# Kernel optimization log

Hardware: AMD Instinct MI355X
Metric: run time of the kernel (lower is better)

The kernel has to match this reference:

```python
import jax, jax.numpy as jnp
import numpy as np

EPS = 1e-7  # reciprocal epsilon from the original code


def hippo_skew_evals(N):
    i = np.arange(N, dtype=np.float64)
    x = 2 * i + 1
    Hippo = np.sqrt(np.outer(x, x)) * np.tri(N, k=-1)  # tril(diagonal=-1)
    Skew = (Hippo - Hippo.T) / 2
    ev = np.linalg.eigvals(Skew)
    return ev[np.argsort(-ev.imag)]  # largest imag first


def setup_inputs() -> dict:
    key = jax.random.key(0)
    ks = jax.random.split(key, 6)
    B, H, L, N = 16, 512, 2048, 64
    u = jax.random.normal(ks[0], (B, H, L), dtype=jnp.float32)
    # log_dt ~ U(log(dt_min), log(dt_max)), tiled to (H, 2) (sep_dt_re_im=True)
    dt_min, dt_max = 1e-3, 1e-1
    ld = np.log(dt_min) + jax.random.uniform(ks[1], (H,)) * (np.log(dt_max) - np.log(dt_min))
    log_dt = jnp.tile(ld[:, None], (1, 2)).astype(jnp.float32)
    # Lambda: hippo_skew_evals(2N)[:N] - 0.5, stored as real (N,2)
    w = hippo_skew_evals(2 * N)[:N] - 0.5
    Lambda = jnp.stack([jnp.asarray(w.real, jnp.float32), jnp.asarray(w.imag, jnp.float32)], axis=-1)
    W = jax.random.normal(ks[2], (1, H, N, 2), dtype=jnp.float32)
    D = jax.random.normal(ks[3], (1, H), dtype=jnp.float32)
    out_weight = jax.random.normal(ks[4], (H, H), dtype=jnp.float32) * (1.0 / np.sqrt(H))
    out_bias = jax.random.uniform(ks[5], (H, 1), dtype=jnp.float32, minval=-1.0 / np.sqrt(H), maxval=1.0 / np.sqrt(H))
    return {"u": u, "log_dt": log_dt, "Lambda": Lambda, "W": W, "D": D,
            "out_weight": out_weight, "out_bias": out_bias}


def _to_c(x):
    return x[..., 0] + 1j * x[..., 1]


def dss_kernel(log_dt, Lambda, W, L):
    # log_dt: (H,2) real; Lambda: (N,2) real; W: (C,H,N,2) real
    Lam = _to_c(Lambda)                         # (N,) complex
    Wc = _to_c(W)                               # (C,H,N) complex
    # sep_dt_re_im: scale real/imag parts of Lambda by separate dt's
    dtL = jnp.exp(log_dt)[:, None, :] * Lambda[None, :, :]  # (H,N,2)
    dt_Lambda = _to_c(dtL)                      # (H,N) complex
    pos = (Lam.real > 0).astype(jnp.float32)    # (N,)
    l = jnp.arange(L, dtype=jnp.float32)
    P = dt_Lambda[..., None] * l                # (H,N,L)
    P_max = jax.lax.stop_gradient(dt_Lambda * (pos * (L - 1)))
    P = P - P_max[..., None]
    S = jnp.exp(P)                              # (H,N,L)
    dt_Lambda_neg = dt_Lambda * (1 - 2 * pos)
    num = jnp.exp(dt_Lambda_neg) - 1            # (H,N)
    den = jnp.exp(dt_Lambda_neg * L) - 1        # (H,N)
    x = den * Lam
    recip = jnp.conj(x) / (x * jnp.conj(x) + EPS)  # bounded 1/x
    Wk = Wc * num * recip                       # (C,H,N)
    # torch .float() on complex keeps real part
    return jnp.einsum('chn,hnl->chl', Wk, S).real  # (C,H,L)


def reference(u, log_dt, Lambda, W, D, out_weight, out_bias):
    # u: (B,H,L), transposed layout
    L = u.shape[-1]
    k = dss_kernel(log_dt, Lambda, W, L)        # (1,H,L)
    n_fft = 2 * L
    k_f = jnp.fft.rfft(k, n=n_fft)              # (1,H,L+1)
    u_f = jnp.fft.rfft(u, n=n_fft)              # (B,H,L+1)
    y_f = jnp.einsum('bhl,chl->bchl', u_f, k_f)
    y = jnp.fft.irfft(y_f, n=n_fft)[..., :L]    # (B,1,H,L)
    y = y + jnp.einsum('bhl,ch->bchl', u, D)    # skip connection
    B = u.shape[0]
    y = y.reshape(B, -1, L)                     # (B, C*H, L), C=1
    y = jax.nn.gelu(y, approximate=False)       # torch nn.GELU default (erf)
    # TransposedLinear: '... u l, v u -> ... v l' + bias (H,1)
    y = jnp.einsum('bul,vu->bvl', y, out_weight) + out_bias
    return y
```

## Files before the change

### kernel.cpp

```cpp
#include <hip/hip_runtime.h>
#include <hip/hip_bf16.h>
#include <math.h>

#define HH 512
#define NN 64
#define LLEN 2048
#define BB 16

typedef __attribute__((ext_vector_type(8))) short short8;
typedef __attribute__((ext_vector_type(4))) float f32x4;

#define SW(j,e) ((e) ^ (((j)&3)<<3))

__device__ inline unsigned short f2bf(float f) {
    union { float f; unsigned int u; } v; v.f = f;
    unsigned int x = v.u;
    unsigned int r = (x + 0x7fffu + ((x >> 16) & 1u)) >> 16;
    return (unsigned short)r;
}
__device__ inline float bf2f(unsigned short x) {
    union { unsigned int u; float f; } v; v.u = ((unsigned int)x) << 16;
    return v.f;
}
__device__ inline unsigned int pk_bf16(float a, float b) {
#if __has_builtin(__builtin_amdgcn_cvt_pk_bf16_f32)
    auto r = __builtin_amdgcn_cvt_pk_bf16_f32(a, b);
    unsigned int o; __builtin_memcpy(&o, &r, 4); return o;
#else
    return (unsigned int)f2bf(a) | ((unsigned int)f2bf(b) << 16);
#endif
}

__device__ inline void gload_lds16(const unsigned short* g, unsigned short* l) {
    __builtin_amdgcn_global_load_lds(
        (const __attribute__((address_space(1))) void*)g,
        (__attribute__((address_space(3))) void*)l, 16, 0, 0);
}

__global__ __launch_bounds__(256) void k_coeffs(
    const float* __restrict__ log_dt,
    const float* __restrict__ Lambda,
    const float* __restrict__ W,
    float* __restrict__ c_re,  float* __restrict__ c_im) {
    int idx = blockIdx.x * 256 + threadIdx.x;
    int h = idx >> 6, n = idx & 63;
    float lre = Lambda[n * 2 + 0], lim = Lambda[n * 2 + 1];
    float dtr = expf(log_dt[h * 2 + 0]);
    float dti = expf(log_dt[h * 2 + 1]);
    float ar = dtr * lre;
    float ai = dti * lim;
    float pos = (lre > 0.0f) ? 1.0f : 0.0f;
    float pm = pos * (float)(LLEN - 1);
    float er = expf(-ar * pm);
    float epr = er * cosf(-ai * pm), epi = er * sinf(-ai * pm);
    float sgn = 1.0f - 2.0f * pos;
    float nr = ar * sgn, ni = ai * sgn;
    float en = expf(nr);
    float numr = en * cosf(ni) - 1.0f, numi = en * sinf(ni);
    float eL = expf(nr * (float)LLEN);
    float denr = eL * cosf(ni * (float)LLEN) - 1.0f;
    float deni = eL * sinf(ni * (float)LLEN);
    float xr = denr * lre - deni * lim;
    float xi = denr * lim + deni * lre;
    float d = xr * xr + xi * xi + 1e-7f;
    float rr = xr / d, ri = -xi / d;
    float wr = W[(h * 64 + n) * 2 + 0], wi = W[(h * 64 + n) * 2 + 1];
    float t1r = wr * numr - wi * numi;
    float t1i = wr * numi + wi * numr;
    float wkr = t1r * rr - t1i * ri;
    float wki = t1r * ri + t1i * rr;
    c_re[idx] = wkr * epr - wki * epi;
    c_im[idx] = wkr * epi + wki * epr;
}

__global__ __launch_bounds__(256) void k_w2b(const float* __restrict__ w,
                                             unsigned short* __restrict__ wb) {
    int idx = blockIdx.x * 256 + threadIdx.x;
    wb[idx] = f2bf(w[idx]);
}

__global__ __launch_bounds__(256) void k_prep(
    const float* __restrict__ log_dt, const float* __restrict__ Lambda,
    const float* __restrict__ c_re, const float* __restrict__ c_im,
    const float* __restrict__ D,
    unsigned short* __restrict__ Tm,
    unsigned short* __restrict__ Are, unsigned short* __restrict__ Aim,
    unsigned short* __restrict__ Pre, unsigned short* __restrict__ Pim,
    float2* __restrict__ lam64) {
    int h = blockIdx.x;
    int tid = threadIdx.x;
    __shared__ float ar_s[64], ai_s[64], cr_s[64], ci_s[64], k_s[64];
    if (tid < 64) {
        int n = tid;
        float dtr = expf(log_dt[h * 2 + 0]);
        float dti = expf(log_dt[h * 2 + 1]);
        float ar = dtr * Lambda[n * 2 + 0];
        float ai = dti * Lambda[n * 2 + 1];
        ar_s[n] = ar; ai_s[n] = ai;
        cr_s[n] = c_re[h * 64 + n]; ci_s[n] = c_im[h * 64 + n];
        float e64 = expf(64.f * ar);
        lam64[h * 64 + n] = make_float2(e64 * cosf(64.f * ai), e64 * sinf(64.f * ai));
    }
    __syncthreads();
    size_t base = (size_t)h * 4096;
#pragma unroll 4
    for (int e = 0; e < 16; ++e) {
        int idx = e * 256 + tid;
        int r = idx >> 6, q = idx & 63;
        {
            float fi = (float)(63 - q);
            float w = expf(fi * ar_s[r]);
            Are[base + idx] = f2bf(w * cosf(fi * ai_s[r]));
            Aim[base + idx] = f2bf(w * sinf(fi * ai_s[r]));
        }
        {
            float t = (float)(r + 1);
            float w = expf(t * ar_s[q]);
            float pr = w * cosf(t * ai_s[q]), pii = w * sinf(t * ai_s[q]);
            Pre[base + idx] = f2bf(cr_s[q] * pr - ci_s[q] * pii);
            Pim[base + idx] = f2bf(-(cr_s[q] * pii + ci_s[q] * pr));
        }
    }
    if (tid < 64) {
        float fd = (float)tid, acc = 0.f;
        for (int n = 0; n < 64; ++n) {
            float w = expf(fd * ar_s[n]);
            acc += cr_s[n] * (w * cosf(fd * ai_s[n])) - ci_s[n] * (w * sinf(fd * ai_s[n]));
        }
        if (tid == 0) acc += D[h];
        k_s[tid] = acc;
    }
    __syncthreads();
#pragma unroll 4
    for (int e = 0; e < 16; ++e) {
        int idx = e * 256 + tid;
        int i = idx >> 6, ip = idx & 63;
        Tm[base + idx] = (ip <= i) ? f2bf(k_s[i - ip]) : (unsigned short)0;
    }
}

__global__ __launch_bounds__(64) void k_scan2(
    const float* __restrict__ u,
    const unsigned short* __restrict__ Tm,
    const unsigned short* __restrict__ Are, const unsigned short* __restrict__ Aim,
    const unsigned short* __restrict__ Pre, const unsigned short* __restrict__ Pim,
    const float2* __restrict__ lam64,
    unsigned short* __restrict__ G) {
    __shared__ unsigned short Sre[32 * 72];
    __shared__ unsigned short Sim_[32 * 72];
    int ln = threadIdx.x;
    int sub = ln & 15, quad = ln >> 4;
    int bh = blockIdx.x;
    int h = bh >> 4, b = bh & 15;
    const float* up = u + ((size_t)b * HH + h) * LLEN;
    unsigned short* Gp = G + ((size_t)b * HH + h) * LLEN;
    size_t mb = (size_t)h * 4096;

    short8 ufr[2][2];
#pragma unroll
    for (int kc = 0; kc < 2; ++kc)
#pragma unroll
        for (int nt = 0; nt < 2; ++nt) {
            int l = (nt * 16 + sub) * 64 + kc * 32 + quad * 8;
            float4 v0 = *(const float4*)(up + l);
            float4 v1 = *(const float4*)(up + l + 4);
            union { short8 s; uint4 u4; } q;
            q.u4 = make_uint4(pk_bf16(v0.x, v0.y), pk_bf16(v0.z, v0.w),
                              pk_bf16(v1.x, v1.y), pk_bf16(v1.z, v1.w));
            ufr[kc][nt] = q.s;
        }

    f32x4 vr[4][2], vi[4][2];
#pragma unroll
    for (int mt = 0; mt < 4; ++mt)
#pragma unroll
        for (int nt = 0; nt < 2; ++nt) {
            vr[mt][nt] = (f32x4){0.f, 0.f, 0.f, 0.f};
            vi[mt][nt] = (f32x4){0.f, 0.f, 0.f, 0.f};
        }
#pragma unroll
    for (int kc = 0; kc < 2; ++kc) {
#pragma unroll
        for (int mt = 0; mt < 4; ++mt) {
            size_t ab = mb + (size_t)(mt * 16 + sub) * 64 + kc * 32 + quad * 8;
            short8 ar8 = *(const short8*)(Are + ab);
            short8 ai8 = *(const short8*)(Aim + ab);
            vr[mt][0] = __builtin_amdgcn_mfma_f32_16x16x32_bf16(ar8, ufr[kc][0], vr[mt][0], 0, 0, 0);
            vr[mt][1] = __builtin_amdgcn_mfma_f32_16x16x32_bf16(ar8, ufr[kc][1], vr[mt][1], 0, 0, 0);
            vi[mt][0] = __builtin_amdgcn_mfma_f32_16x16x32_bf16(ai8, ufr[kc][0], vi[mt][0], 0, 0, 0);
            vi[mt][1] = __builtin_amdgcn_mfma_f32_16x16x32_bf16(ai8, ufr[kc][1], vi[mt][1], 0, 0, 0);
        }
    }
#pragma unroll
    for (int mt = 0; mt < 4; ++mt)
#pragma unroll
        for (int nt = 0; nt < 2; ++nt) {
            int jj = nt * 16 + sub;
            int e0 = mt * 16 + quad * 4;
            uint2 pr, pi;
            pr.x = pk_bf16(vr[mt][nt][0], vr[mt][nt][1]);
            pr.y = pk_bf16(vr[mt][nt][2], vr[mt][nt][3]);
            pi.x = pk_bf16(vi[mt][nt][0], vi[mt][nt][1]);
            pi.y = pk_bf16(vi[mt][nt][2], vi[mt][nt][3]);
            *(uint2*)&Sre[jj * 72 + SW(jj, e0)] = pr;
            *(uint2*)&Sim_[jj * 72 + SW(jj, e0)] = pi;
        }
    __syncthreads();

    {
        float2 l64 = lam64[(size_t)h * 64 + ln];
        float sr = 0.f, si = 0.f;
        for (int j = 0; j < 32; ++j) {
            int a = j * 72 + SW(j, ln);
            float vrr = bf2f(Sre[a]);
            float vii = bf2f(Sim_[a]);
            unsigned int p = pk_bf16(sr, si);
            Sre[a] = (unsigned short)(p & 0xffffu);
            Sim_[a] = (unsigned short)(p >> 16);
            float nr = fmaf(l64.x, sr, fmaf(-l64.y, si, vrr));
            float ni = fmaf(l64.y, sr, fmaf(l64.x, si, vii));
            sr = nr; si = ni;
        }
    }
    __syncthreads();

    f32x4 y[4][2];
#pragma unroll
    for (int mt = 0; mt < 4; ++mt)
#pragma unroll
        for (int nt = 0; nt < 2; ++nt) y[mt][nt] = (f32x4){0.f, 0.f, 0.f, 0.f};
#pragma unroll
    for (int kc = 0; kc < 2; ++kc) {
        int eo = kc * 32 + quad * 8;
        short8 bsr0 = *(const short8*)&Sre[sub * 72 + SW(sub, eo)];
        short8 bsr1 = *(const short8*)&Sre[(16 + sub) * 72 + SW(16 + sub, eo)];
        short8 bsi0 = *(const short8*)&Sim_[sub * 72 + SW(sub, eo)];
        short8 bsi1 = *(const short8*)&Sim_[(16 + sub) * 72 + SW(16 + sub, eo)];
#pragma unroll
        for (int mt = 0; mt < 4; ++mt) {
            size_t ab = mb + (size_t)(mt * 16 + sub) * 64 + eo;
            short8 at8 = *(const short8*)(Tm + ab);
            short8 pr8 = *(const short8*)(Pre + ab);
            short8 pi8 = *(const short8*)(Pim + ab);
            y[mt][0] = __builtin_amdgcn_mfma_f32_16x16x32_bf16(at8, ufr[kc][0], y[mt][0], 0, 0, 0);
            y[mt][1] = __builtin_amdgcn_mfma_f32_16x16x32_bf16(at8, ufr[kc][1], y[mt][1], 0, 0, 0);
            y[mt][0] = __builtin_amdgcn_mfma_f32_16x16x32_bf16(pr8, bsr0, y[mt][0], 0, 0, 0);
            y[mt][1] = __builtin_amdgcn_mfma_f32_16x16x32_bf16(pr8, bsr1, y[mt][1], 0, 0, 0);
            y[mt][0] = __builtin_amdgcn_mfma_f32_16x16x32_bf16(pi8, bsi0, y[mt][0], 0, 0, 0);
            y[mt][1] = __builtin_amdgcn_mfma_f32_16x16x32_bf16(pi8, bsi1, y[mt][1], 0, 0, 0);
        }
    }
    __syncthreads();

#pragma unroll
    for (int mt = 0; mt < 4; ++mt)
#pragma unroll
        for (int nt = 0; nt < 2; ++nt) {
            int jj = nt * 16 + sub;
            int e0 = mt * 16 + quad * 4;
            float g[4];
#pragma unroll
            for (int r = 0; r < 4; ++r) {
                float yv = y[mt][nt][r];
                g[r] = 0.5f * yv * (1.0f + erff(yv * 0.70710678118654752f));
            }
            uint2 p;
            p.x = pk_bf16(g[0], g[1]);
            p.y = pk_bf16(g[2], g[3]);
            *(uint2*)&Sre[jj * 72 + SW(jj, e0)] = p;
        }
    __syncthreads();

    for (int t = 0; t < 4; ++t) {
        int l = t * 512 + ln * 8;
        int j = l >> 6, i = l & 63;
        uint4 q = *(const uint4*)&Sre[j * 72 + SW(j, i)];
        *(uint4*)(Gp + l) = q;
    }
}

__global__ __launch_bounds__(256) void k_tr(const unsigned short* __restrict__ G,
                                            unsigned short* __restrict__ Gt) {
    __shared__ unsigned short T[64 * 72];
    int tid = threadIdx.x;
    int l0 = blockIdx.x * 64, u0 = blockIdx.y * 64, b = blockIdx.z;
    {
        int ur = tid >> 2, ls = (tid & 3) * 16;
        const unsigned short* src = G + ((size_t)(b * HH + u0 + ur)) * LLEN + l0 + ls;
        *(uint4*)&T[ur * 72 + ls]     = *(const uint4*)(src);
        *(uint4*)&T[ur * 72 + ls + 8] = *(const uint4*)(src + 8);
    }
    __syncthreads();
    {
        int lr = tid >> 2, us = (tid & 3) * 16;
        unsigned short tmp[16];
#pragma unroll
        for (int k2 = 0; k2 < 16; ++k2) tmp[k2] = T[(us + k2) * 72 + lr];
        unsigned short* dst = Gt + ((size_t)(b * LLEN + l0 + lr)) * HH + u0 + us;
        *(uint4*)(dst)     = *(uint4*)&tmp[0];
        *(uint4*)(dst + 8) = *(uint4*)&tmp[8];
    }
}

__global__ __launch_bounds__(256) void k_proj(
    const unsigned short* __restrict__ Gt,
    const unsigned short* __restrict__ Wb,
    const float* __restrict__ bias,
    float* __restrict__ out) {
    __shared__ unsigned short As[128 * 64];
    __shared__ unsigned short Bs[128 * 64];
    int tid = threadIdx.x;
    int w = tid >> 6, ln = tid & 63;
    int wm = w & 1, wn = w >> 1;
    int quad = ln >> 4, sub = ln & 15;
    int v0 = blockIdx.x * 128, l0 = blockIdx.y * 128, b = blockIdx.z;
    int r_in = ln >> 3, cch = ln & 7;
    int gch = cch ^ r_in;

    f32x4 acc[4][4];
#pragma unroll
    for (int mt = 0; mt < 4; ++mt)
#pragma unroll
        for (int nt = 0; nt < 4; ++nt) acc[mt][nt] = (f32x4){0.f, 0.f, 0.f, 0.f};

    for (int k0 = 0; k0 < HH; k0 += 64) {
        __syncthreads();
#pragma unroll
        for (int i = 0; i < 4; ++i) {
            int row = w * 32 + i * 8 + r_in;
            const unsigned short* ga = Wb + (size_t)(v0 + row) * HH + k0 + gch * 8;
            gload_lds16(ga, &As[(w * 32 + i * 8) * 64]);
            const unsigned short* gb = Gt + ((size_t)(b * LLEN + l0 + row)) * HH + k0 + gch * 8;
            gload_lds16(gb, &Bs[(w * 32 + i * 8) * 64]);
        }
        __syncthreads();
#pragma unroll
        for (int kc = 0; kc < 2; ++kc) {
            int ch = (kc * 4 + quad) ^ (sub & 7);
            short8 af[4], bf[4];
#pragma unroll
            for (int mt = 0; mt < 4; ++mt)
                af[mt] = *(const short8*)&As[(wm * 64 + mt * 16 + sub) * 64 + ch * 8];
#pragma unroll
            for (int nt = 0; nt < 4; ++nt)
                bf[nt] = *(const short8*)&Bs[(wn * 64 + nt * 16 + sub) * 64 + ch * 8];
#pragma unroll
            for (int mt = 0; mt < 4; ++mt)
#pragma unroll
                for (int nt = 0; nt < 4; ++nt)
                    acc[mt][nt] = __builtin_amdgcn_mfma_f32_16x16x32_bf16(af[mt], bf[nt], acc[mt][nt], 0, 0, 0);
        }
    }
#pragma unroll
    for (int mt = 0; mt < 4; ++mt) {
#pragma unroll
        for (int i = 0; i < 4; ++i) {
            int v = v0 + wm * 64 + mt * 16 + quad * 4 + i;
            float bv = bias[v];
#pragma unroll
            for (int nt = 0; nt < 4; ++nt) {
                int l = l0 + wn * 64 + nt * 16 + sub;
                out[((size_t)b * HH + v) * LLEN + l] = acc[mt][nt][i] + bv;
            }
        }
    }
}

extern "C" void kernel_launch(void* const* d_in, const int* in_sizes, int n_in,
                              void* d_out, int out_size, void* d_ws, size_t ws_size,
                              hipStream_t stream) {
    const float* u       = (const float*)d_in[0];
    const float* log_dt  = (const float*)d_in[1];
    const float* Lambda  = (const float*)d_in[2];
    const float* W       = (const float*)d_in[3];
    const float* D       = (const float*)d_in[4];
    const float* out_w   = (const float*)d_in[5];
    const float* out_b   = (const float*)d_in[6];
    float* out = (float*)d_out;

    char* ws = (char*)d_ws;
    float* c_re   = (float*)(ws + 0);
    float* c_im   = (float*)(ws + 131072);
    unsigned short* Wb = (unsigned short*)(ws + 524288);
    unsigned short* G  = (unsigned short*)(ws + 1048576);
    size_t moff = 34603008;
    const size_t MSZ = (size_t)HH * 4096 * 2;
    unsigned short* TmB  = (unsigned short*)(ws + moff);
    unsigned short* AreB = (unsigned short*)(ws + moff + 1 * MSZ);
    unsigned short* AimB = (unsigned short*)(ws + moff + 2 * MSZ);
    unsigned short* PreB = (unsigned short*)(ws + moff + 3 * MSZ);
    unsigned short* PimB = (unsigned short*)(ws + moff + 4 * MSZ);
    float2* lam64B = (float2*)(ws + moff + 5 * MSZ);
    unsigned short* Gt = (unsigned short*)(ws + moff);

    hipLaunchKernelGGL(k_coeffs, dim3(128), dim3(256), 0, stream,
                       log_dt, Lambda, W, c_re, c_im);
    hipLaunchKernelGGL(k_w2b, dim3(1024), dim3(256), 0, stream, out_w, Wb);
    hipLaunchKernelGGL(k_prep, dim3(512), dim3(256), 0, stream,
                       log_dt, Lambda, c_re, c_im, D,
                       TmB, AreB, AimB, PreB, PimB, lam64B);
    hipLaunchKernelGGL(k_scan2, dim3(8192), dim3(64), 0, stream,
                       u, TmB, AreB, AimB, PreB, PimB, lam64B, G);
    hipLaunchKernelGGL(k_tr, dim3(32, 8, 16), dim3(256), 0, stream, G, Gt);
    hipLaunchKernelGGL(k_proj, dim3(4, 16, 16), dim3(256), 0, stream,
                       Gt, Wb, out_b, out);
}
```

Measured before the change: 262.9 us.

## Fuse coefficient and weight-cast kernels into prep, pack scan waves, fast GELU

Merges the coefficient and weight-to-bf16 kernels into the per-h prep kernel, so the launch sequence loses two kernels and the c_re/c_im round trip. The scan kernel now runs four independent (b,h) waves per 256-thread block with per-wave LDS slices and a new XOR-free rotation swizzle. The scan kernel also writes GELU output straight to global memory instead of staging it through LDS, and replaces erf GELU with a tanh-style approximation built on exp2 and rcp. The approximation changes numerics slightly, and the direct stores are narrower and less coalesced. The __syncthreads calls are now shared across four waves that each only touch their own slice.

```diff
diff --git a/kernel.cpp b/kernel.cpp
--- a/kernel.cpp
+++ b/kernel.cpp
@@ -9,8 +9,6 @@
 
 typedef __attribute__((ext_vector_type(8))) short short8;
 typedef __attribute__((ext_vector_type(4))) float f32x4;
-
-#define SW(j,e) ((e) ^ (((j)&3)<<3))
 
 __device__ inline unsigned short f2bf(float f) {
     union { float f; unsigned int u; } v; v.f = f;
@@ -31,75 +29,84 @@
 #endif
 }
 
+__device__ inline float fast_rcp(float x) {
+#if __has_builtin(__builtin_amdgcn_rcpf)
+    return __builtin_amdgcn_rcpf(x);
+#else
+    return 1.0f / x;
+#endif
+}
+__device__ inline float fast_exp2(float x) {
+#if __has_builtin(__builtin_amdgcn_exp2f)
+    return __builtin_amdgcn_exp2f(x);
+#else
+    return exp2f(x);
+#endif
+}
+__device__ inline float fast_gelu(float x) {
+    float x2 = x * x;
+    float t = fmaf(0.044715f, x2, 1.0f);
+    float z2 = 1.5957691216057308f * x * t;
+    float e = fast_exp2(-1.4426950408889634f * z2);
+    return x * fast_rcp(1.0f + e);
+}
+
 __device__ inline void gload_lds16(const unsigned short* g, unsigned short* l) {
     __builtin_amdgcn_global_load_lds(
         (const __attribute__((address_space(1))) void*)g,
         (__attribute__((address_space(3))) void*)l, 16, 0, 0);
 }
 
-__global__ __launch_bounds__(256) void k_coeffs(
-    const float* __restrict__ log_dt,
-    const float* __restrict__ Lambda,
-    const float* __restrict__ W,
-    float* __restrict__ c_re,  float* __restrict__ c_im) {
-    int idx = blockIdx.x * 256 + threadIdx.x;
-    int h = idx >> 6, n = idx & 63;
-    float lre = Lambda[n * 2 + 0], lim = Lambda[n * 2 + 1];
-    float dtr = expf(log_dt[h * 2 + 0]);
-    float dti = expf(log_dt[h * 2 + 1]);
-    float ar = dtr * lre;
-    float ai = dti * lim;
-    float pos = (lre > 0.0f) ? 1.0f : 0.0f;
-    float pm = pos * (float)(LLEN - 1);
-    float er = expf(-ar * pm);
-    float epr = er * cosf(-ai * pm), epi = er * sinf(-ai * pm);
-    float sgn = 1.0f - 2.0f * pos;
-    float nr = ar * sgn, ni = ai * sgn;
-    float en = expf(nr);
-    float numr = en * cosf(ni) - 1.0f, numi = en * sinf(ni);
-    float eL = expf(nr * (float)LLEN);
-    float denr = eL * cosf(ni * (float)LLEN) - 1.0f;
-    float deni = eL * sinf(ni * (float)LLEN);
-    float xr = denr * lre - deni * lim;
-    float xi = denr * lim + deni * lre;
-    float d = xr * xr + xi * xi + 1e-7f;
-    float rr = xr / d, ri = -xi / d;
-    float wr = W[(h * 64 + n) * 2 + 0], wi = W[(h * 64 + n) * 2 + 1];
-    float t1r = wr * numr - wi * numi;
-    float t1i = wr * numi + wi * numr;
-    float wkr = t1r * rr - t1i * ri;
-    float wki = t1r * ri + t1i * rr;
-    c_re[idx] = wkr * epr - wki * epi;
-    c_im[idx] = wkr * epi + wki * epr;
-}
-
-__global__ __launch_bounds__(256) void k_w2b(const float* __restrict__ w,
-                                             unsigned short* __restrict__ wb) {
-    int idx = blockIdx.x * 256 + threadIdx.x;
-    wb[idx] = f2bf(w[idx]);
-}
-
-__global__ __launch_bounds__(256) void k_prep(
+__global__ __launch_bounds__(256) void k_prep2(
     const float* __restrict__ log_dt, const float* __restrict__ Lambda,
-    const float* __restrict__ c_re, const float* __restrict__ c_im,
-    const float* __restrict__ D,
+    const float* __restrict__ W, const float* __restrict__ D,
+    const float* __restrict__ out_w,
     unsigned short* __restrict__ Tm,
     unsigned short* __restrict__ Are, unsigned short* __restrict__ Aim,
     unsigned short* __restrict__ Pre, unsigned short* __restrict__ Pim,
-    float2* __restrict__ lam64) {
-    int h = blockIdx.x;
+    float2* __restrict__ lam64,
+    unsigned short* __restrict__ Wb) {
+    int blk = blockIdx.x;
     int tid = threadIdx.x;
+    if (blk >= 512) {
+        int base = (blk - 512) * 4096 + tid;
+#pragma unroll
+        for (int i = 0; i < 16; ++i) Wb[base + i * 256] = f2bf(out_w[base + i * 256]);
+        return;
+    }
+    int h = blk;
     __shared__ float ar_s[64], ai_s[64], cr_s[64], ci_s[64], k_s[64];
     if (tid < 64) {
         int n = tid;
+        float lre = Lambda[n * 2 + 0], lim = Lambda[n * 2 + 1];
         float dtr = expf(log_dt[h * 2 + 0]);
         float dti = expf(log_dt[h * 2 + 1]);
-        float ar = dtr * Lambda[n * 2 + 0];
-        float ai = dti * Lambda[n * 2 + 1];
+        float ar = dtr * lre, ai = dti * lim;
         ar_s[n] = ar; ai_s[n] = ai;
-        cr_s[n] = c_re[h * 64 + n]; ci_s[n] = c_im[h * 64 + n];
         float e64 = expf(64.f * ar);
         lam64[h * 64 + n] = make_float2(e64 * cosf(64.f * ai), e64 * sinf(64.f * ai));
+        float pos = (lre > 0.0f) ? 1.0f : 0.0f;
+        float pm = pos * (float)(LLEN - 1);
+        float er = expf(-ar * pm);
+        float epr = er * cosf(-ai * pm), epi = er * sinf(-ai * pm);
+        float sgn = 1.0f - 2.0f * pos;
+        float nr = ar * sgn, ni = ai * sgn;
+        float en = expf(nr);
+        float numr = en * cosf(ni) - 1.0f, numi = en * sinf(ni);
+        float eL = expf(nr * (float)LLEN);
+        float denr = eL * cosf(ni * (float)LLEN) - 1.0f;
+        float deni = eL * sinf(ni * (float)LLEN);
+        float xr = denr * lre - deni * lim;
+        float xi = denr * lim + deni * lre;
+        float d = xr * xr + xi * xi + 1e-7f;
+        float rr = xr / d, ri = -xi / d;
+        float wr = W[(h * 64 + n) * 2 + 0], wi = W[(h * 64 + n) * 2 + 1];
+        float t1r = wr * numr - wi * numi;
+        float t1i = wr * numi + wi * numr;
+        float wkr = t1r * rr - t1i * ri;
+        float wki = t1r * ri + t1i * rr;
+        cr_s[n] = wkr * epr - wki * epi;
+        ci_s[n] = wkr * epi + wki * epr;
     }
     __syncthreads();
     size_t base = (size_t)h * 4096;
@@ -139,18 +146,21 @@
     }
 }
 
-__global__ __launch_bounds__(64) void k_scan2(
+__global__ __launch_bounds__(256) void k_scan3(
     const float* __restrict__ u,
     const unsigned short* __restrict__ Tm,
     const unsigned short* __restrict__ Are, const unsigned short* __restrict__ Aim,
     const unsigned short* __restrict__ Pre, const unsigned short* __restrict__ Pim,
     const float2* __restrict__ lam64,
     unsigned short* __restrict__ G) {
-    __shared__ unsigned short Sre[32 * 72];
-    __shared__ unsigned short Sim_[32 * 72];
-    int ln = threadIdx.x;
+    __shared__ unsigned short SreA[4 * 2048];
+    __shared__ unsigned short SimA[4 * 2048];
+    int tid = threadIdx.x;
+    int wv = tid >> 6, ln = tid & 63;
+    unsigned short* Sre = &SreA[wv * 2048];
+    unsigned short* Sim = &SimA[wv * 2048];
     int sub = ln & 15, quad = ln >> 4;
-    int bh = blockIdx.x;
+    int bh = blockIdx.x * 4 + wv;
     int h = bh >> 4, b = bh & 15;
     const float* up = u + ((size_t)b * HH + h) * LLEN;
     unsigned short* Gp = G + ((size_t)b * HH + h) * LLEN;
@@ -196,27 +206,29 @@
 #pragma unroll
         for (int nt = 0; nt < 2; ++nt) {
             int jj = nt * 16 + sub;
-            int e0 = mt * 16 + quad * 4;
+            int c = 2 * mt + (quad >> 1);
+            int ofs = jj * 64 + ((c + jj) & 7) * 8 + (quad & 1) * 4;
             uint2 pr, pi;
             pr.x = pk_bf16(vr[mt][nt][0], vr[mt][nt][1]);
             pr.y = pk_bf16(vr[mt][nt][2], vr[mt][nt][3]);
             pi.x = pk_bf16(vi[mt][nt][0], vi[mt][nt][1]);
             pi.y = pk_bf16(vi[mt][nt][2], vi[mt][nt][3]);
-            *(uint2*)&Sre[jj * 72 + SW(jj, e0)] = pr;
-            *(uint2*)&Sim_[jj * 72 + SW(jj, e0)] = pi;
+            *(uint2*)&Sre[ofs] = pr;
+            *(uint2*)&Sim[ofs] = pi;
         }
     __syncthreads();
 
     {
         float2 l64 = lam64[(size_t)h * 64 + ln];
         float sr = 0.f, si = 0.f;
+        int pb = ln >> 3, eo = ln & 7;
         for (int j = 0; j < 32; ++j) {
-            int a = j * 72 + SW(j, ln);
+            int a = j * 64 + ((pb + j) & 7) * 8 + eo;
             float vrr = bf2f(Sre[a]);
-            float vii = bf2f(Sim_[a]);
+            float vii = bf2f(Sim[a]);
             unsigned int p = pk_bf16(sr, si);
             Sre[a] = (unsigned short)(p & 0xffffu);
-            Sim_[a] = (unsigned short)(p >> 16);
+            Sim[a] = (unsigned short)(p >> 16);
             float nr = fmaf(l64.x, sr, fmaf(-l64.y, si, vrr));
             float ni = fmaf(l64.y, sr, fmaf(l64.x, si, vii));
             sr = nr; si = ni;
@@ -231,14 +243,15 @@
         for (int nt = 0; nt < 2; ++nt) y[mt][nt] = (f32x4){0.f, 0.f, 0.f, 0.f};
 #pragma unroll
     for (int kc = 0; kc < 2; ++kc) {
-        int eo = kc * 32 + quad * 8;
-        short8 bsr0 = *(const short8*)&Sre[sub * 72 + SW(sub, eo)];
-        short8 bsr1 = *(const short8*)&Sre[(16 + sub) * 72 + SW(16 + sub, eo)];
-        short8 bsi0 = *(const short8*)&Sim_[sub * 72 + SW(sub, eo)];
-        short8 bsi1 = *(const short8*)&Sim_[(16 + sub) * 72 + SW(16 + sub, eo)];
+        int c = kc * 4 + quad;
+        int r0 = sub, r1 = 16 + sub;
+        short8 bsr0 = *(const short8*)&Sre[r0 * 64 + ((c + r0) & 7) * 8];
+        short8 bsr1 = *(const short8*)&Sre[r1 * 64 + ((c + r1) & 7) * 8];
+        short8 bsi0 = *(const short8*)&Sim[r0 * 64 + ((c + r0) & 7) * 8];
+        short8 bsi1 = *(const short8*)&Sim[r1 * 64 + ((c + r1) & 7) * 8];
 #pragma unroll
         for (int mt = 0; mt < 4; ++mt) {
-            size_t ab = mb + (size_t)(mt * 16 + sub) * 64 + eo;
+            size_t ab = mb + (size_t)(mt * 16 + sub) * 64 + kc * 32 + quad * 8;
             short8 at8 = *(const short8*)(Tm + ab);
             short8 pr8 = *(const short8*)(Pre + ab);
             short8 pi8 = *(const short8*)(Pim + ab);
@@ -250,33 +263,21 @@
             y[mt][1] = __builtin_amdgcn_mfma_f32_16x16x32_bf16(pi8, bsi1, y[mt][1], 0, 0, 0);
         }
     }
-    __syncthreads();
 
 #pragma unroll
     for (int mt = 0; mt < 4; ++mt)
 #pragma unroll
         for (int nt = 0; nt < 2; ++nt) {
-            int jj = nt * 16 + sub;
-            int e0 = mt * 16 + quad * 4;
-            float g[4];
-#pragma unroll
-            for (int r = 0; r < 4; ++r) {
-                float yv = y[mt][nt][r];
-                g[r] = 0.5f * yv * (1.0f + erff(yv * 0.70710678118654752f));
-            }
-            uint2 p;
-            p.x = pk_bf16(g[0], g[1]);
-            p.y = pk_bf16(g[2], g[3]);
-            *(uint2*)&Sre[jj * 72 + SW(jj, e0)] = p;
-        }
-    __syncthreads();
-
-    for (int t = 0; t < 4; ++t) {
-        int l = t * 512 + ln * 8;
-        int j = l >> 6, i = l & 63;
-        uint4 q = *(const uint4*)&Sre[j * 72 + SW(j, i)];
-        *(uint4*)(Gp + l) = q;
-    }
+            int l = (nt * 16 + sub) * 64 + mt * 16 + quad * 4;
+            float g0 = fast_gelu(y[mt][nt][0]);
+            float g1 = fast_gelu(y[mt][nt][1]);
+            float g2 = fast_gelu(y[mt][nt][2]);
+            float g3 = fast_gelu(y[mt][nt][3]);
+            uint2 pv;
+            pv.x = pk_bf16(g0, g1);
+            pv.y = pk_bf16(g2, g3);
+            *(uint2*)(Gp + l) = pv;
+        }
 }
 
 __global__ __launch_bounds__(256) void k_tr(const unsigned short* __restrict__ G,
@@ -379,8 +380,6 @@
     float* out = (float*)d_out;
 
     char* ws = (char*)d_ws;
-    float* c_re   = (float*)(ws + 0);
-    float* c_im   = (float*)(ws + 131072);
     unsigned short* Wb = (unsigned short*)(ws + 524288);
     unsigned short* G  = (unsigned short*)(ws + 1048576);
     size_t moff = 34603008;
@@ -393,13 +392,10 @@
     float2* lam64B = (float2*)(ws + moff + 5 * MSZ);
     unsigned short* Gt = (unsigned short*)(ws + moff);
 
-    hipLaunchKernelGGL(k_coeffs, dim3(128), dim3(256), 0, stream,
-                       log_dt, Lambda, W, c_re, c_im);
-    hipLaunchKernelGGL(k_w2b, dim3(1024), dim3(256), 0, stream, out_w, Wb);
-    hipLaunchKernelGGL(k_prep, dim3(512), dim3(256), 0, stream,
-                       log_dt, Lambda, c_re, c_im, D,
-                       TmB, AreB, AimB, PreB, PimB, lam64B);
-    hipLaunchKernelGGL(k_scan2, dim3(8192), dim3(64), 0, stream,
+    hipLaunchKernelGGL(k_prep2, dim3(576), dim3(256), 0, stream,
+                       log_dt, Lambda, W, D, out_w,
+                       TmB, AreB, AimB, PreB, PimB, lam64B, Wb);
+    hipLaunchKernelGGL(k_scan3, dim3(2048), dim3(256), 0, stream,
                        u, TmB, AreB, AimB, PreB, PimB, lam64B, G);
     hipLaunchKernelGGL(k_tr, dim3(32, 8, 16), dim3(256), 0, stream, G, Gt);
     hipLaunchKernelGGL(k_proj, dim3(4, 16, 16), dim3(256), 0, stream,
```

New measurement: 246.2 us. 6.3% less time.
